# Kernel optimization log

Measured on AMD Instinct MI355X. Metric: run time of the kernel, lower is better.

Reference implementation:

```python
import jax, jax.numpy as jnp
import numpy as np

DIM = 64
SQRT_DIM = np.sqrt(DIM).astype(np.float32)
NEG_INF = -1e9


def setup_inputs() -> dict:
    key = jax.random.key(0)
    kq, kk, kv, km = jax.random.split(key, 4)
    B, Q, K, D = 32, 1024, 1024, DIM
    query = jax.random.normal(kq, (B, Q, D), dtype=jnp.float32)
    k = jax.random.normal(kk, (B, K, D), dtype=jnp.float32)
    value = jax.random.normal(kv, (B, K, D), dtype=jnp.float32)
    mask = jax.random.randint(km, (B, Q, K), 0, 2).astype(jnp.bool_)
    return {"query": query, "key": k, "value": value, "mask": mask}


def reference(query, key, value, mask):
    # score: [B, Q, K]
    score = jnp.einsum('bqd,bkd->bqk', query, key) / SQRT_DIM
    score = jnp.where(mask, NEG_INF, score)
    attn = jax.nn.softmax(score, axis=-1)
    context = jnp.einsum('bqk,bkd->bqd', attn, value)
    return (context, attn)
```

## Files before the change

kernel.cpp:

```cpp
#include <hip/hip_runtime.h>

constexpr int BATCH = 32;
constexpr int QLEN  = 1024;
constexpr int KLEN  = 1024;
constexpr int DIM   = 64;
constexpr int TQ    = 16;

typedef float    f32x4 __attribute__((ext_vector_type(4)));
typedef int      i32x4 __attribute__((ext_vector_type(4)));
typedef _Float16 f16x8 __attribute__((ext_vector_type(8)));
typedef _Float16 f16x4 __attribute__((ext_vector_type(4)));
typedef unsigned long long u64;
typedef unsigned int u32;

__device__ __forceinline__ f16x8 cvt_h8(f32x4 a, f32x4 b) {
  f16x8 h;
  h[0] = (_Float16)a[0]; h[1] = (_Float16)a[1]; h[2] = (_Float16)a[2]; h[3] = (_Float16)a[3];
  h[4] = (_Float16)b[0]; h[5] = (_Float16)b[1]; h[6] = (_Float16)b[2]; h[7] = (_Float16)b[3];
  return h;
}

constexpr int TK = 128;
__global__ __launch_bounds__(256)
void vtkh_kernel(const float* __restrict__ V, const float* __restrict__ Kg,
                 _Float16* __restrict__ Vt, _Float16* __restrict__ Kh) {
  __shared__ _Float16 lt[DIM][TK + 8];
  const int b = blockIdx.y, k0 = blockIdx.x * TK;
  const int t = threadIdx.x;
  const int d4 = (t & 15) * 4;
  #pragma unroll
  for (int p = 0; p < TK / 16; ++p) {
    const int kl = (t >> 4) + p * 16;
    const f32x4 v = *(const f32x4*)(V + ((size_t)(b * KLEN + k0 + kl)) * DIM + d4);
    #pragma unroll
    for (int j = 0; j < 4; ++j) lt[d4 + j][kl] = (_Float16)v[j];
  }
  #pragma unroll
  for (int p = 0; p < 8; ++p) {
    const int idx = t + p * 256;
    const int kl = idx >> 4, dd = (idx & 15) * 4;
    const f32x4 v = *(const f32x4*)(Kg + ((size_t)(b * KLEN + k0 + kl)) * DIM + dd);
    f16x4 h = { (_Float16)v[0], (_Float16)v[1], (_Float16)v[2], (_Float16)v[3] };
    *(f16x4*)(Kh + ((size_t)(b * KLEN + k0 + kl)) * DIM + dd) = h;
  }
  __syncthreads();
  const int d = t >> 2;
  #pragma unroll
  for (int j2 = 0; j2 < TK / 32; ++j2) {
    const int seg = (t & 3) + j2 * 4;
    *(f16x8*)(Vt + (size_t)b * DIM * KLEN + (size_t)d * KLEN + k0 + seg * 8) =
        *(const f16x8*)(&lt[d][seg * 8]);
  }
}

__global__ __launch_bounds__(256, 2)
void sdpa_kernel(const float* __restrict__ Qg, const _Float16* __restrict__ Kh,
                 const _Float16* __restrict__ Vt, const int* __restrict__ Mg,
                 float* __restrict__ Ctx, float* __restrict__ Attn)
{
  __shared__ float rs[2][4][16];
  __shared__ __attribute__((aligned(16))) _Float16 sp[2][TQ * 1024];

  const int tid  = threadIdx.x;
  const int w    = tid >> 6;
  const int l    = tid & 63;
  const int n16  = l & 15;
  const int quad = l >> 4;

  const int base = blockIdx.x * 4;

  i32x4 mv[16];

  auto loadMask = [&](int lin) {
    const int b = lin >> 6, q0 = (lin & 63) * TQ;
    const int* mrow = Mg + ((size_t)(b * QLEN + q0 + n16)) * KLEN + w * 256 + quad * 4;
    #pragma unroll
    for (int tt = 0; tt < 16; ++tt)
      mv[tt] = __builtin_nontemporal_load((const i32x4*)(mrow + tt * 16));
  };

  auto computeA = [&](int lin, int buf) {
    const int b = lin >> 6, q0 = (lin & 63) * TQ;
    char* const spb = (char*)&sp[buf][0];
    const float qscl = 0.125f * 1.44269504f;
    const float* qb = Qg + ((size_t)(b * QLEN + q0 + n16)) * DIM + quad * 8;
    f32x4 qa0 = *(const f32x4*)(qb),      qa1 = *(const f32x4*)(qb + 4);
    f32x4 qa2 = *(const f32x4*)(qb + 32), qa3 = *(const f32x4*)(qb + 36);
    #pragma unroll
    for (int i = 0; i < 4; ++i) { qa0[i] *= qscl; qa1[i] *= qscl; qa2[i] *= qscl; qa3[i] *= qscl; }
    const f16x8 aq0 = cvt_h8(qa0, qa1);
    const f16x8 aq1 = cvt_h8(qa2, qa3);
    const _Float16* kb = Kh + (size_t)b * KLEN * DIM + quad * 8;
    f32x4 rsum4 = {0.f, 0.f, 0.f, 0.f};
    #pragma unroll
    for (int tt = 0; tt < 16; ++tt) {
      const _Float16* kp = kb + (size_t)((w * 16 + tt) * 16 + n16) * DIM;
      const f16x8 ak0 = *(const f16x8*)(kp);
      const f16x8 ak1 = *(const f16x8*)(kp + 32);
      f32x4 acc = {0.f, 0.f, 0.f, 0.f};
      acc = __builtin_amdgcn_mfma_f32_16x16x32_f16(ak0, aq0, acc, 0, 0, 0);
      acc = __builtin_amdgcn_mfma_f32_16x16x32_f16(ak1, aq1, acc, 0, 0, 0);
      f16x4 ph;
      #pragma unroll
      for (int i = 0; i < 4; ++i) {
        const float e = mv[tt][i] ? 0.f : __builtin_amdgcn_exp2f(acc[i]);
        rsum4[i] += e;
        ph[i] = (_Float16)e;
      }
      const int g = w * 64 + tt * 4 + quad;
      *(f16x4*)(spb + (n16 << 11) + ((g * 8) ^ ((n16 & 7) << 4))) = ph;
    }
    float rsum = (rsum4[0] + rsum4[1]) + (rsum4[2] + rsum4[3]);
    rsum += __shfl_xor(rsum, 16, 64);
    rsum += __shfl_xor(rsum, 32, 64);
    if (quad == 0) rs[buf][w][n16] = rsum;
  };

  auto passC = [&](int lin, int buf) {
    const int b = lin >> 6, q0 = (lin & 63) * TQ;
    char* const spb = (char*)&sp[buf][0];
    #pragma unroll
    for (int rr = 0; rr < 4; ++rr) {
      const int row = w * 4 + rr;
      const float invr = __builtin_amdgcn_rcpf(
          rs[buf][0][row] + rs[buf][1][row] + rs[buf][2][row] + rs[buf][3][row]);
      float* arow = Attn + ((size_t)(b * QLEN + q0 + row)) * KLEN;
      #pragma unroll
      for (int j = 0; j < 4; ++j) {
        const int g = j * 64 + l;
        const f16x4 hv = *(const f16x4*)(spb + (row << 11) + ((g * 8) ^ ((row & 7) << 4)));
        f32x4 ov = { (float)hv[0] * invr, (float)hv[1] * invr,
                     (float)hv[2] * invr, (float)hv[3] * invr };
        *(f32x4*)(arow + j * 256 + l * 4) = ov;
      }
    }
    const _Float16* vtb = Vt + ((size_t)(b * DIM + w * 16 + n16)) * KLEN;
    f32x4 c0 = {0.f, 0.f, 0.f, 0.f}, c1 = {0.f, 0.f, 0.f, 0.f};
    #pragma unroll 8
    for (int m = 0; m < 32; m += 2) {
      const int ga = m * 8 + quad * 2;
      const f16x8 pa0 = *(const f16x8*)(spb + (n16 << 11) + ((ga * 8) ^ ((n16 & 7) << 4)));
      const f16x8 pa1 = *(const f16x8*)(spb + (n16 << 11) + (((ga + 8) * 8) ^ ((n16 & 7) << 4)));
      const f16x8 bv0 = *(const f16x8*)(vtb + m * 32 + quad * 8);
      const f16x8 bv1 = *(const f16x8*)(vtb + (m + 1) * 32 + quad * 8);
      c0 = __builtin_amdgcn_mfma_f32_16x16x32_f16(bv0, pa0, c0, 0, 0, 0);
      c1 = __builtin_amdgcn_mfma_f32_16x16x32_f16(bv1, pa1, c1, 0, 0, 0);
    }
    const float invq = __builtin_amdgcn_rcpf(
        rs[buf][0][n16] + rs[buf][1][n16] + rs[buf][2][n16] + rs[buf][3][n16]);
    f32x4 cv = { (c0[0] + c1[0]) * invq, (c0[1] + c1[1]) * invq,
                 (c0[2] + c1[2]) * invq, (c0[3] + c1[3]) * invq };
    *(f32x4*)(Ctx + ((size_t)(b * QLEN + q0 + n16)) * DIM + w * 16 + quad * 4) = cv;
  };

  loadMask(base);
  computeA(base, 0);
  __syncthreads();
  #pragma unroll
  for (int t = 0; t < 4; ++t) {
    const int cur = t & 1;
    if (t < 3) loadMask(base + t + 1);
    passC(base + t, cur);
    if (t < 3) {
      computeA(base + t + 1, cur ^ 1);
      __syncthreads();
    }
  }
}

extern "C" void kernel_launch(void* const* d_in, const int* in_sizes, int n_in,
                              void* d_out, int out_size, void* d_ws, size_t ws_size,
                              hipStream_t stream) {
  const float* Qg = (const float*)d_in[0];
  const float* Kg = (const float*)d_in[1];
  const float* Vg = (const float*)d_in[2];
  const int*   Mg = (const int*)d_in[3];
  float* Ctx  = (float*)d_out;
  float* Attn = (float*)d_out + (size_t)BATCH * QLEN * DIM;
  _Float16* Vt = (_Float16*)d_ws;
  _Float16* Kh = (_Float16*)((char*)d_ws + (size_t)BATCH * DIM * KLEN * 2);

  dim3 tgrid(KLEN / TK, BATCH);
  vtkh_kernel<<<tgrid, 256, 0, stream>>>(Vg, Kg, Vt, Kh);

  sdpa_kernel<<<512, 256, 0, stream>>>(Qg, Kh, Vt, Mg, Ctx, Attn);
}
```

Baseline: 308.3 us.

## Pack attention mask into bitmask in a separate pre-pass kernel

Adds a kernel that reads the int32 mask once and packs it into 64-bit ballot words laid out to match the MFMA tile lanes. The attention kernel then loads four u64 words per lane instead of sixteen i32x4 vectors, which drops 64 mask registers and most of its global mask traffic. The cost is an extra launch and a separate bandwidth-bound pass over the full 128MB mask that no longer overlaps with compute. It also needs more workspace for the packed mask.

Result: no change. 304.8 us (-1.1%).

```diff
diff --git a/kernel.cpp b/kernel.cpp
--- a/kernel.cpp
+++ b/kernel.cpp
@@ -12,6 +12,7 @@
 typedef _Float16 f16x4 __attribute__((ext_vector_type(4)));
 typedef unsigned long long u64;
 typedef unsigned int u32;
+typedef u64 u64x4 __attribute__((ext_vector_type(4)));
 
 __device__ __forceinline__ f16x8 cvt_h8(f32x4 a, f32x4 b) {
   f16x8 h;
@@ -53,9 +54,29 @@
   }
 }
 
+__global__ __launch_bounds__(256)
+void maskpack_kernel(const int* __restrict__ Mg, u64* __restrict__ Mp) {
+  const int l  = threadIdx.x & 63;
+  const int gw = blockIdx.x * 4 + (threadIdx.x >> 6);
+  for (int row = gw; row < BATCH * QLEN; row += 8192) {
+    const int* mr = Mg + (size_t)row * KLEN;
+    u64 myw = 0;
+    #pragma unroll
+    for (int c = 0; c < 4; ++c) {
+      const i32x4 v = __builtin_nontemporal_load((const i32x4*)(mr + c * 256 + l * 4));
+      #pragma unroll
+      for (int u = 0; u < 4; ++u) {
+        const u64 bl = __ballot(v[u] != 0);
+        if (l == c * 4 + u) myw = bl;
+      }
+    }
+    if (l < 16) Mp[(size_t)row * 16 + l] = myw;
+  }
+}
+
 __global__ __launch_bounds__(256, 2)
 void sdpa_kernel(const float* __restrict__ Qg, const _Float16* __restrict__ Kh,
-                 const _Float16* __restrict__ Vt, const int* __restrict__ Mg,
+                 const _Float16* __restrict__ Vt, const u64* __restrict__ Mp,
                  float* __restrict__ Ctx, float* __restrict__ Attn)
 {
   __shared__ float rs[2][4][16];
@@ -69,14 +90,11 @@
 
   const int base = blockIdx.x * 4;
 
-  i32x4 mv[16];
+  u64x4 mw;
 
   auto loadMask = [&](int lin) {
     const int b = lin >> 6, q0 = (lin & 63) * TQ;
-    const int* mrow = Mg + ((size_t)(b * QLEN + q0 + n16)) * KLEN + w * 256 + quad * 4;
-    #pragma unroll
-    for (int tt = 0; tt < 16; ++tt)
-      mv[tt] = __builtin_nontemporal_load((const i32x4*)(mrow + tt * 16));
+    mw = *(const u64x4*)(Mp + ((size_t)(b * QLEN + q0 + n16)) * 16 + w * 4);
   };
 
   auto computeA = [&](int lin, int buf) {
@@ -100,10 +118,12 @@
       f32x4 acc = {0.f, 0.f, 0.f, 0.f};
       acc = __builtin_amdgcn_mfma_f32_16x16x32_f16(ak0, aq0, acc, 0, 0, 0);
       acc = __builtin_amdgcn_mfma_f32_16x16x32_f16(ak1, aq1, acc, 0, 0, 0);
+      const u32 sh = tt * 4 + quad;
       f16x4 ph;
       #pragma unroll
       for (int i = 0; i < 4; ++i) {
-        const float e = mv[tt][i] ? 0.f : __builtin_amdgcn_exp2f(acc[i]);
+        const float e = ((mw[i] >> sh) & 1ULL) ? 0.f
+                          : __builtin_amdgcn_exp2f(acc[i]);
         rsum4[i] += e;
         ph[i] = (_Float16)e;
       }
@@ -177,11 +197,16 @@
   const int*   Mg = (const int*)d_in[3];
   float* Ctx  = (float*)d_out;
   float* Attn = (float*)d_out + (size_t)BATCH * QLEN * DIM;
-  _Float16* Vt = (_Float16*)d_ws;
-  _Float16* Kh = (_Float16*)((char*)d_ws + (size_t)BATCH * DIM * KLEN * 2);
+
+  char* ws = (char*)d_ws;
+  _Float16* Vt = (_Float16*)ws;
+  _Float16* Kh = (_Float16*)(ws + (size_t)4 * 1024 * 1024);
+  u64*      Mp = (u64*)     (ws + (size_t)8 * 1024 * 1024);
 
   dim3 tgrid(KLEN / TK, BATCH);
   vtkh_kernel<<<tgrid, 256, 0, stream>>>(Vg, Kg, Vt, Kh);
 
-  sdpa_kernel<<<512, 256, 0, stream>>>(Qg, Kh, Vt, Mg, Ctx, Attn);
-}
+  maskpack_kernel<<<2048, 256, 0, stream>>>(Mg, Mp);
+
+  sdpa_kernel<<<512, 256, 0, stream>>>(Qg, Kh, Vt, Mp, Ctx, Attn);
+}
```
